# Kernel optimization log

Measured on AMD Instinct MI355X. Metric: run time of the kernel, lower is better.

The kernel has to match this reference:

```python
import jax, jax.numpy as jnp
import numpy as np

FL = 320       # frame length
FS = 80        # frame shift
ORDER = 16     # poly order (a[0] == 1)
EMPH = 0.97    # pre/de-emphasis coefficient


def setup_inputs() -> dict:
    key = jax.random.key(0)
    k1, k2 = jax.random.split(key)
    B, F = 64, 3000
    L = F * FS  # 240000
    excit = jax.random.normal(k1, (B, L, 1), dtype=jnp.float32) * 0.1
    # LPC coefficients: a[0] = 1, remaining taps small for numerical stability
    rest = jax.random.normal(k2, (B, F, ORDER - 1), dtype=jnp.float32) * (0.3 / (ORDER - 1))
    lpc_coef = jnp.concatenate([jnp.ones((B, F, 1), jnp.float32), rest], axis=-1)
    return {"excit": excit, "lpc_coef": lpc_coef}


def reference(excit, lpc_coef):
    """LPCSynthesisPytorch: AR synthesis recursion followed by de-emphasis.

    excit:    (B, L, 1)
    lpc_coef: (B, F, order), a[0] assumed 1, L = F * FS
    returns:  (B, L, 1)
    """
    B, L, _ = excit.shape
    order = lpc_coef.shape[-1]

    # Per-sample AR taps a[1:], expanded frame->sample, time-major for scan.
    a = jnp.repeat(lpc_coef[:, :, 1:], FS, axis=1)[:, :L]      # (B, L, order-1)
    a_t = jnp.transpose(a, (1, 0, 2))                          # (L, B, order-1)
    e_t = jnp.transpose(excit[..., 0], (1, 0))                 # (L, B)

    def ar_step(buf, inp):
        # buf: (B, order-1) = [x[n-order+1], ..., x[n-1]] (last entry most recent)
        a_n, e_n = inp
        # predicted = sum_k a[k] * x[n-k]; output = excit - predicted
        pre = -jnp.sum(a_n * buf[:, ::-1], axis=-1)
        out = e_n + pre
        buf = jnp.concatenate([buf[:, 1:], out[:, None]], axis=-1)
        return buf, out

    buf0 = jnp.zeros((B, order - 1), dtype=excit.dtype)
    _, y_t = jax.lax.scan(ar_step, buf0, (a_t, e_t))           # (L, B)

    # De-emphasis IIR: z[n] = y[n] + EMPH * z[n-1], z[-1] = 0
    def deemph_step(prev, x):
        cur = x + EMPH * prev
        return cur, cur

    _, z_t = jax.lax.scan(deemph_step, jnp.zeros((B,), excit.dtype), y_t)
    return jnp.transpose(z_t, (1, 0))[..., None]               # (B, L, 1)
```

## Files before the change

kernel.cpp:

```cpp
#include <hip/hip_runtime.h>


namespace {
constexpr int kHS = 40;
constexpr int kF = 3000;
constexpr int kH = 2 * kF;
constexpr int kL = kHS * kH;
constexpr int kOrder = 16;
constexpr int kB = 64;
constexpr float kEmph = 0.97f;
constexpr int kThreads = 128;
constexpr int kJunk = 9;
constexpr int kEmitH = kThreads - kJunk;
constexpr int kSlotF = 42;
constexpr int kCols = 51;
constexpr float kLg97 = -4.3943347e-2f;
constexpr float kR1 = 0.2957118f;
constexpr float kR2 = 0.08744547f;
constexpr float kR3 = 0.02585867f;
constexpr float kR4 = 0.00764671f;
constexpr float kR5 = 0.00226126f;
constexpr float kR6 = 6.6867e-4f;
constexpr float kR7 = 1.9773e-4f;
constexpr float kR8 = 5.8472e-5f;

typedef float vfloat4 __attribute__((ext_vector_type(4)));
typedef float vfloat2 __attribute__((ext_vector_type(2)));
}

#define AR_SAMPLE(A, s, e_in, ACC)                                         \
  float ACC;                                                               \
  {                                                                        \
    float t0 = (e_in);                                                     \
    t0 = fmaf(-A[14], x[((s)-15) & 15], t0);                               \
    t0 = fmaf(-A[13], x[((s)-14) & 15], t0);                               \
    t0 = fmaf(-A[12], x[((s)-13) & 15], t0);                               \
    t0 = fmaf(-A[11], x[((s)-12) & 15], t0);                               \
    t0 = fmaf(-A[10], x[((s)-11) & 15], t0);                               \
    float t1 = -A[9] * x[((s)-10) & 15];                                   \
    t1 = fmaf(-A[8], x[((s)-9) & 15], t1);                                 \
    t1 = fmaf(-A[7], x[((s)-8) & 15], t1);                                 \
    t1 = fmaf(-A[6], x[((s)-7) & 15], t1);                                 \
    t1 = fmaf(-A[5], x[((s)-6) & 15], t1);                                 \
    float t2 = -A[4] * x[((s)-5) & 15];                                    \
    t2 = fmaf(-A[3], x[((s)-4) & 15], t2);                                 \
    t2 = fmaf(-A[2], x[((s)-3) & 15], t2);                                 \
    t2 = fmaf(-A[1], x[((s)-2) & 15], t2);                                 \
    const float t01 = t0 + t1;                      \
    t2 = fmaf(-A[0], x[((s)-1) & 15], t2);            \
    ACC = t01 + t2;                                           \
    x[(s)&15] = ACC;                                                       \
  }

__global__ __launch_bounds__(kThreads) void lpc_synth_kernel(
    const float* __restrict__ excit, const float* __restrict__ coef,
    float* __restrict__ out) {
  __shared__ float s_z[kThreads * kSlotF];
  __shared__ float s_zend[kThreads];
  __shared__ float s_zp[kThreads];

  const int tid = threadIdx.x;
  const int b = blockIdx.y;
  const int hbase = blockIdx.x * kEmitH;
  const int ht = hbase + tid - kJunk;
  const int hc = min(max(ht, 0), kH - 1);
  const int h1 = min(max(ht - 1, 0), kH - 1);
  const int h2 = min(max(ht - 2, 0), kH - 1);

  const float* __restrict__ ebase = excit + (size_t)b * kL;
  const float* __restrict__ cbase = coef + (size_t)b * kF * kOrder;

  const vfloat4* __restrict__ cp_ =
      (const vfloat4*)(cbase + (size_t)(h2 >> 1) * kOrder);
  const vfloat4* __restrict__ cc_ =
      (const vfloat4*)(cbase + (size_t)(hc >> 1) * kOrder);
  const vfloat4 p0 = cp_[0], p1 = cp_[1], p2 = cp_[2], p3 = cp_[3];
  const vfloat4 q0 = cc_[0], q1 = cc_[1], q2 = cc_[2], q3 = cc_[3];

  float pa_[15] = {p0.y, p0.z, p0.w, p1.x, p1.y, p1.z, p1.w, p2.x,
                   p2.y, p2.z, p2.w, p3.x, p3.y, p3.z, p3.w};
  const float ca_[15] = {q0.y, q0.z, q0.w, q1.x, q1.y, q1.z, q1.w, q2.x,
                         q2.y, q2.z, q2.w, q3.x, q3.y, q3.z, q3.w};

  float x[16];
#pragma unroll
  for (int i = 0; i < 16; ++i) x[i] = 0.f;

  {
    const vfloat4* __restrict__ e2 = (const vfloat4*)(ebase + h2 * kHS);
    const vfloat4* __restrict__ e1 = (const vfloat4*)(ebase + h1 * kHS);
    const float m2 = (ht >= 2) ? 1.f : 0.f;
    const float m1 = (ht >= 1) ? 1.f : 0.f;
#pragma unroll
    for (int j = 8; j < 10; ++j) {
      const vfloat4 v = e2[j];
      const float f_[4] = {m2 * v.x, m2 * v.y, m2 * v.z, m2 * v.w};
#pragma unroll
      for (int q = 0; q < 4; ++q) {
        AR_SAMPLE(pa_, 4 * (j - 8) + q, f_[q], acc)
        (void)acc;
      }
    }
    if (ht & 1) {
#pragma unroll
      for (int k = 0; k < 15; ++k) pa_[k] = ca_[k];
    }
#pragma unroll
    for (int j = 0; j < 10; ++j) {
      const vfloat4 v = e1[j];
      const float f_[4] = {m1 * v.x, m1 * v.y, m1 * v.z, m1 * v.w};
#pragma unroll
      for (int q = 0; q < 4; ++q) {
        AR_SAMPLE(pa_, 8 + 4 * j + q, f_[q], acc)
        (void)acc;
      }
    }
  }

  float z = 0.f;
  {
    const vfloat4* __restrict__ ee_ = (const vfloat4*)(ebase + hc * kHS);
    float* __restrict__ so = s_z + tid * kSlotF;
#pragma unroll
    for (int j = 0; j < 10; ++j) {
      const vfloat4 v = ee_[j];
      float zv[4];
#pragma unroll
      for (int q = 0; q < 4; ++q) {
        AR_SAMPLE(ca_, 48 + 4 * j + q, v[q], acc)
        z = fmaf(kEmph, z, acc);
        zv[q] = z;
      }
      vfloat2 a, c;
      a.x = zv[0]; a.y = zv[1];
      c.x = zv[2]; c.y = zv[3];
      *(vfloat2*)(so + 4 * j) = a;
      *(vfloat2*)(so + 4 * j + 2) = c;
    }
  }
  s_zend[tid] = (ht < 0 || ht >= kH) ? 0.f : z;
  __syncthreads();

  if (tid < kEmitH) {
    float Zp = s_zend[tid + 8];
    Zp = fmaf(kR1, s_zend[tid + 7], Zp);
    Zp = fmaf(kR2, s_zend[tid + 6], Zp);
    Zp = fmaf(kR3, s_zend[tid + 5], Zp);
    Zp = fmaf(kR4, s_zend[tid + 4], Zp);
    Zp = fmaf(kR5, s_zend[tid + 3], Zp);
    Zp = fmaf(kR6, s_zend[tid + 2], Zp);
    Zp = fmaf(kR7, s_zend[tid + 1], Zp);
    Zp = fmaf(kR8, s_zend[tid + 0], Zp);
    s_zp[tid] = Zp;
  }
  __syncthreads();

  {
    const int nv4 = min(kEmitH, kH - hbase) * 10;
    vfloat4* __restrict__ ob =
        (vfloat4*)(out + (size_t)b * kL + (size_t)hbase * kHS);
#pragma unroll 1
    for (int i = tid; i < nv4; i += kThreads) {
      const int k = i / 10;
      const int j = i - 10 * k;
      const float* sp = s_z + (k + kJunk) * kSlotF + 4 * j;
      const vfloat2 h0 = *(const vfloat2*)sp;
      const vfloat2 h1v = *(const vfloat2*)(sp + 2);
      const float Zp = s_zp[k];
      const float ee = __builtin_exp2f(kLg97 * (float)(4 * j + 1));
      vfloat4 v;
      v.x = fmaf(ee, Zp, h0.x);
      v.y = fmaf(ee * 0.97f, Zp, h0.y);
      v.z = fmaf(ee * 0.9409f, Zp, h1v.x);
      v.w = fmaf(ee * 0.912673f, Zp, h1v.y);
      ob[i] = v;
    }
  }
}
#undef AR_SAMPLE

extern "C" void kernel_launch(void* const* d_in, const int* in_sizes, int n_in,
                              void* d_out, int out_size, void* d_ws,
                              size_t ws_size, hipStream_t stream) {
  const float* excit = (const float*)d_in[0];
  const float* coef = (const float*)d_in[1];
  float* out = (float*)d_out;

  dim3 grid(kCols, kB);
  lpc_synth_kernel<<<grid, kThreads, 0, stream>>>(excit, coef, out);
}
```

Before: 136.8 us.

## Stage excitation tile in shared memory with coalesced loads and reuse

Loads the block's excitation window (130 slots of 40 samples) from global memory into shared memory with coalesced vfloat4 loads, instead of each thread reading three overlapping half-frames directly from global memory. The warm-up and main AR passes then read from shared memory, and the main pass writes its de-emphasised output back into the same slots in place. Slots are padded to 44 floats so 16-byte vector accesses are possible. This cuts the redundant global traffic and uncoalesced per-thread strided reads, at the cost of an extra barrier and more shared memory per block.

```diff
diff --git a/kernel.cpp b/kernel.cpp
--- a/kernel.cpp
+++ b/kernel.cpp
@@ -6,13 +6,16 @@
 constexpr int kF = 3000;
 constexpr int kH = 2 * kF;
 constexpr int kL = kHS * kH;
+constexpr int kL4 = kL / 4;
 constexpr int kOrder = 16;
 constexpr int kB = 64;
 constexpr float kEmph = 0.97f;
 constexpr int kThreads = 128;
 constexpr int kJunk = 9;
 constexpr int kEmitH = kThreads - kJunk;
-constexpr int kSlotF = 42;
+constexpr int kInSlots = 130;
+constexpr int kSlotW = 44;
+constexpr int kIn4 = kInSlots * 10;
 constexpr int kCols = 51;
 constexpr float kLg97 = -4.3943347e-2f;
 constexpr float kR1 = 0.2957118f;
@@ -25,7 +28,6 @@
 constexpr float kR8 = 5.8472e-5f;
 
 typedef float vfloat4 __attribute__((ext_vector_type(4)));
-typedef float vfloat2 __attribute__((ext_vector_type(2)));
 }
 
 #define AR_SAMPLE(A, s, e_in, ACC)                                         \
@@ -55,7 +57,7 @@
 __global__ __launch_bounds__(kThreads) void lpc_synth_kernel(
     const float* __restrict__ excit, const float* __restrict__ coef,
     float* __restrict__ out) {
-  __shared__ float s_z[kThreads * kSlotF];
+  __shared__ float s_x[kInSlots * kSlotW];
   __shared__ float s_zend[kThreads];
   __shared__ float s_zp[kThreads];
 
@@ -63,37 +65,61 @@
   const int b = blockIdx.y;
   const int hbase = blockIdx.x * kEmitH;
   const int ht = hbase + tid - kJunk;
-  const int hc = min(max(ht, 0), kH - 1);
-  const int h1 = min(max(ht - 1, 0), kH - 1);
-  const int h2 = min(max(ht - 2, 0), kH - 1);
 
   const float* __restrict__ ebase = excit + (size_t)b * kL;
   const float* __restrict__ cbase = coef + (size_t)b * kF * kOrder;
 
+  {
+  }
+  const int hcT = min(max(ht, 0), kH - 1);
+  const int hwT = min(max(ht - 2, 0), kH - 1);
   const vfloat4* __restrict__ cp_ =
-      (const vfloat4*)(cbase + (size_t)(h2 >> 1) * kOrder);
+      (const vfloat4*)(cbase + (size_t)(hwT >> 1) * kOrder);
   const vfloat4* __restrict__ cc_ =
-      (const vfloat4*)(cbase + (size_t)(hc >> 1) * kOrder);
+      (const vfloat4*)(cbase + (size_t)(hcT >> 1) * kOrder);
   const vfloat4 p0 = cp_[0], p1 = cp_[1], p2 = cp_[2], p3 = cp_[3];
   const vfloat4 q0 = cc_[0], q1 = cc_[1], q2 = cc_[2], q3 = cc_[3];
+
+  {
+    const vfloat4* __restrict__ eg = (const vfloat4*)ebase;
+    const int base4 = (hbase - 11) * 10;
+#pragma unroll
+    for (int p = 0; p < 10; ++p) {
+      const int i = tid + p * kThreads;
+      const int g4 = min(max(base4 + i, 0), kL4 - 1);
+      const vfloat4 v = eg[g4];
+      const int slot = i / 10;
+      const int o = i - slot * 10;
+      *(vfloat4*)(s_x + slot * kSlotW + o * 4) = v;
+    }
+    if (tid < kIn4 - 10 * kThreads) {
+      const int i = 10 * kThreads + tid;
+      const int g4 = min(max(base4 + i, 0), kL4 - 1);
+      const vfloat4 v = eg[g4];
+      const int slot = i / 10;
+      const int o = i - slot * 10;
+      *(vfloat4*)(s_x + slot * kSlotW + o * 4) = v;
+    }
+  }
+  __syncthreads();
+
+  float x[16];
+#pragma unroll
+  for (int i = 0; i < 16; ++i) x[i] = 0.f;
 
   float pa_[15] = {p0.y, p0.z, p0.w, p1.x, p1.y, p1.z, p1.w, p2.x,
                    p2.y, p2.z, p2.w, p3.x, p3.y, p3.z, p3.w};
   const float ca_[15] = {q0.y, q0.z, q0.w, q1.x, q1.y, q1.z, q1.w, q2.x,
                          q2.y, q2.z, q2.w, q3.x, q3.y, q3.z, q3.w};
 
-  float x[16];
-#pragma unroll
-  for (int i = 0; i < 16; ++i) x[i] = 0.f;
-
-  {
-    const vfloat4* __restrict__ e2 = (const vfloat4*)(ebase + h2 * kHS);
-    const vfloat4* __restrict__ e1 = (const vfloat4*)(ebase + h1 * kHS);
+  {
+    const float* __restrict__ s2 = s_x + tid * kSlotW;
+    const float* __restrict__ s1 = s_x + (tid + 1) * kSlotW;
     const float m2 = (ht >= 2) ? 1.f : 0.f;
     const float m1 = (ht >= 1) ? 1.f : 0.f;
 #pragma unroll
     for (int j = 8; j < 10; ++j) {
-      const vfloat4 v = e2[j];
+      const vfloat4 v = *(const vfloat4*)(s2 + 4 * j);
       const float f_[4] = {m2 * v.x, m2 * v.y, m2 * v.z, m2 * v.w};
 #pragma unroll
       for (int q = 0; q < 4; ++q) {
@@ -107,7 +133,7 @@
     }
 #pragma unroll
     for (int j = 0; j < 10; ++j) {
-      const vfloat4 v = e1[j];
+      const vfloat4 v = *(const vfloat4*)(s1 + 4 * j);
       const float f_[4] = {m1 * v.x, m1 * v.y, m1 * v.z, m1 * v.w};
 #pragma unroll
       for (int q = 0; q < 4; ++q) {
@@ -116,26 +142,25 @@
       }
     }
   }
+  __syncthreads();
 
   float z = 0.f;
   {
-    const vfloat4* __restrict__ ee_ = (const vfloat4*)(ebase + hc * kHS);
-    float* __restrict__ so = s_z + tid * kSlotF;
+    float* __restrict__ so = s_x + (tid + 2) * kSlotW;
 #pragma unroll
     for (int j = 0; j < 10; ++j) {
-      const vfloat4 v = ee_[j];
-      float zv[4];
+      const vfloat4 v = *(const vfloat4*)(so + 4 * j);
+      vfloat4 zv;
 #pragma unroll
       for (int q = 0; q < 4; ++q) {
         AR_SAMPLE(ca_, 48 + 4 * j + q, v[q], acc)
         z = fmaf(kEmph, z, acc);
-        zv[q] = z;
+        if (q == 0) zv.x = z;
+        if (q == 1) zv.y = z;
+        if (q == 2) zv.z = z;
+        if (q == 3) zv.w = z;
       }
-      vfloat2 a, c;
-      a.x = zv[0]; a.y = zv[1];
-      c.x = zv[2]; c.y = zv[3];
-      *(vfloat2*)(so + 4 * j) = a;
-      *(vfloat2*)(so + 4 * j + 2) = c;
+      *(vfloat4*)(so + 4 * j) = zv;
     }
   }
   s_zend[tid] = (ht < 0 || ht >= kH) ? 0.f : z;
@@ -163,16 +188,14 @@
     for (int i = tid; i < nv4; i += kThreads) {
       const int k = i / 10;
       const int j = i - 10 * k;
-      const float* sp = s_z + (k + kJunk) * kSlotF + 4 * j;
-      const vfloat2 h0 = *(const vfloat2*)sp;
-      const vfloat2 h1v = *(const vfloat2*)(sp + 2);
+      const vfloat4 h = *(const vfloat4*)(s_x + (k + 11) * kSlotW + 4 * j);
       const float Zp = s_zp[k];
       const float ee = __builtin_exp2f(kLg97 * (float)(4 * j + 1));
       vfloat4 v;
-      v.x = fmaf(ee, Zp, h0.x);
-      v.y = fmaf(ee * 0.97f, Zp, h0.y);
-      v.z = fmaf(ee * 0.9409f, Zp, h1v.x);
-      v.w = fmaf(ee * 0.912673f, Zp, h1v.y);
+      v.x = fmaf(ee, Zp, h.x);
+      v.y = fmaf(ee * 0.97f, Zp, h.y);
+      v.z = fmaf(ee * 0.9409f, Zp, h.z);
+      v.w = fmaf(ee * 0.912673f, Zp, h.w);
       ob[i] = v;
     }
   }
```

After: 124.8 us. 8.8% less time.
